# Kernel tuning notes

Measured on AMD Instinct MI355X. Metric: run time of the kernel, lower is better.

## Reference

```python
import jax, jax.numpy as jnp
import numpy as np

D_MODEL = 1024
NUM_HEADS = 16
D_K = D_MODEL // NUM_HEADS


def setup_inputs() -> dict:
    key = jax.random.key(0)
    ks = jax.random.split(key, 8)
    B, S = 2, 2048
    std = 1.0 / np.sqrt(D_MODEL)
    return {
        "Q": jax.random.normal(ks[0], (B, S, D_MODEL), jnp.float32),
        "K": jax.random.normal(ks[1], (B, S, D_MODEL), jnp.float32),
        "V": jax.random.normal(ks[2], (B, S, D_MODEL), jnp.float32),
        "W_q": jax.random.normal(ks[3], (D_MODEL, D_MODEL), jnp.float32) * std,
        "W_k": jax.random.normal(ks[4], (D_MODEL, D_MODEL), jnp.float32) * std,
        "W_v": jax.random.normal(ks[5], (D_MODEL, D_MODEL), jnp.float32) * std,
        "W_o": jax.random.normal(ks[6], (D_MODEL, D_MODEL), jnp.float32) * std,
        "b_o": jnp.zeros((D_MODEL,), jnp.float32),
    }


def reference(Q, K, V, W_q, W_k, W_v, W_o, b_o):
    B, S, _ = Q.shape
    H, dk = NUM_HEADS, D_K
    scale = 1.0 / np.sqrt(dk)
    # project and split heads: [B, H, S, dk]
    def split_heads(x, W):
        return (x @ W.T).reshape(B, -1, H, dk).transpose(0, 2, 1, 3)
    q = split_heads(Q, W_q)
    k = split_heads(K, W_k)
    v = split_heads(V, W_v)
    # scores: [B, H, S, S]
    scores = jnp.einsum("bhqd,bhkd->bhqk", q, k) * scale
    causal_mask = jnp.triu(jnp.ones((S, S), bool), k=1)
    scores = jnp.where(causal_mask, -jnp.inf, scores)
    attn = jax.nn.softmax(scores, axis=-1)
    out = jnp.einsum("bhqk,bhkd->bhqd", attn, v)  # [B, H, S, dk]
    out = out.transpose(0, 2, 1, 3).reshape(B, S, H * dk)
    out = out @ W_o.T + b_o
    return out, attn
```

## Files before the change

kernel.cpp:

```cpp
#include <hip/hip_runtime.h>
#include <hip/hip_bf16.h>

#define SEQ 2048
#define BATCH 2
#define NH 16
#define DK 64
#define DM 1024

typedef __bf16 bf16;
typedef __bf16 bf16x8 __attribute__((ext_vector_type(8)));
typedef float f32x4 __attribute__((ext_vector_type(4)));
typedef short s16x4 __attribute__((ext_vector_type(4)));

#define MFMA16(a,b,c) __builtin_amdgcn_mfma_f32_16x16x32_bf16(a,b,c,0,0,0)
#define NEG_BIG (-1.0e30f)

#define GLL16(gsrc, ldst) __builtin_amdgcn_global_load_lds( \
    (const __attribute__((address_space(1))) void*)(gsrc), \
    (__attribute__((address_space(3))) void*)(ldst), 16, 0, 0)

__device__ __forceinline__ bf16x8 ld8(const bf16* p){ return *(const bf16x8*)p; }

__device__ __forceinline__ bf16x8 frag_bf16lds(const bf16* Ls, int row, int lq){
    int c = lq ^ (row&3);
    return *(const bf16x8*)((const char*)Ls + row*64 + c*16);
}

__global__ __launch_bounds__(256) void cvt_kernel(
    const float* __restrict__ Q,  const float* __restrict__ K,  const float* __restrict__ V,
    const float* __restrict__ Wq, const float* __restrict__ Wk, const float* __restrict__ Wv,
    bf16* __restrict__ Qb, bf16* __restrict__ Kb, bf16* __restrict__ Vb,
    bf16* __restrict__ Wqb, bf16* __restrict__ Wkb, bf16* __restrict__ Wvb)
{
    const int a = blockIdx.y;
    const float* src = (a==0)?Q:(a==1)?K:(a==2)?V:(a==3)?Wq:(a==4)?Wk:Wv;
    bf16* dst        = (a==0)?Qb:(a==1)?Kb:(a==2)?Vb:(a==3)?Wqb:(a==4)?Wkb:Wvb;
    const int n4 = (a<3) ? (BATCH*SEQ*DM)/4 : (DM*DM)/4;
    for (int i = blockIdx.x*256 + threadIdx.x; i < n4; i += gridDim.x*256){
        f32x4 v = ((const f32x4*)src)[i];
        bf16 o[4];
        #pragma unroll
        for (int j=0;j<4;j++) o[j] = (bf16)v[j];
        ((s16x4*)dst)[i] = *(const s16x4*)o;
    }
}

__global__ __launch_bounds__(256) void cvtW_kernel(
    const float* __restrict__ W, bf16* __restrict__ Wb)
{
    const int n4 = (DM*DM)/4;
    for (int i = blockIdx.x*256 + threadIdx.x; i < n4; i += gridDim.x*256){
        f32x4 v = ((const f32x4*)W)[i];
        bf16 o[4];
        #pragma unroll
        for (int j=0;j<4;j++) o[j] = (bf16)v[j];
        ((s16x4*)Wb)[i] = *(const s16x4*)o;
    }
}

__device__ __forceinline__ void gemm_tile_bf16(
    const bf16* __restrict__ X, const bf16* __restrict__ W,
    bf16* As, bf16* Bs, int m0, int n0, int tid, int mt, int nt0,
    int lr, int lq, f32x4 acc[4][4])
{
    for (int k0 = 0; k0 < DM; k0 += 32) {
        if (k0) __syncthreads();
        #pragma unroll
        for (int i=0;i<2;i++){
            int ci  = i*256 + tid;
            int row = ci >> 2, ch = ci & 3;
            int gc  = (ch ^ (row&3)) << 3;
            GLL16(X + (size_t)(m0+row)*DM + k0 + gc, (char*)As + ci*16);
            GLL16(W + (size_t)(n0+row)*DM + k0 + gc, (char*)Bs + ci*16);
        }
        __syncthreads();
        bf16x8 af[4], bfr[4];
        #pragma unroll
        for (int mi=0;mi<4;mi++) af[mi]  = frag_bf16lds(As, mt  + mi*16 + lr, lq);
        #pragma unroll
        for (int ni=0;ni<4;ni++) bfr[ni] = frag_bf16lds(Bs, nt0 + ni*16 + lr, lq);
        #pragma unroll
        for (int mi=0;mi<4;mi++)
            #pragma unroll
            for (int ni=0;ni<4;ni++)
                acc[mi][ni] = MFMA16(af[mi], bfr[ni], acc[mi][ni]);
    }
}

__global__ __launch_bounds__(256) void qkv_proj_kernel(
    const bf16* __restrict__ Qb, const bf16* __restrict__ Kb, const bf16* __restrict__ Vb,
    const bf16* __restrict__ Wqb, const bf16* __restrict__ Wkb, const bf16* __restrict__ Wvb,
    bf16* __restrict__ q_s, bf16* __restrict__ k_s, bf16* __restrict__ vt_s)
{
    __shared__ __align__(16) bf16 As[128*32];
    __shared__ __align__(16) bf16 Bs[128*32];
    const int z = blockIdx.z;
    const bf16* X = (z==0) ? Qb  : (z==1) ? Kb  : Vb;
    const bf16* W = (z==0) ? Wqb : (z==1) ? Wkb : Wvb;
    bf16* out     = (z==0) ? q_s : (z==1) ? k_s : vt_s;

    const int tid  = threadIdx.x;
    const int lane = tid & 63;
    const int w    = tid >> 6;
    const int lr = lane & 15, lq = lane >> 4;
    const int mt  = (w>>1)*64;
    const int nt0 = (w&1)*64;
    const int m0 = blockIdx.y*128;
    const int n0 = blockIdx.x*128;

    f32x4 acc[4][4] = {};
    gemm_tile_bf16(X, W, As, Bs, m0, n0, tid, mt, nt0, lr, lq, acc);

    if (z == 2) {
        #pragma unroll
        for (int mi=0;mi<4;mi++)
        #pragma unroll
        for (int ni=0;ni<4;ni++){
            int row = m0 + mt + mi*16 + lq*4;
            int col = n0 + nt0 + ni*16 + lr;
            int b = row >> 11, s = row & (SEQ-1);
            int h = col >> 6,  dd = col & 63;
            bf16 pk[4];
            #pragma unroll
            for (int r=0;r<4;r++) pk[r] = (bf16)acc[mi][ni][r];
            *(s16x4*)&out[((size_t)((b*NH + h)*DK + dd))*SEQ + s] = *(const s16x4*)pk;
        }
    } else {
        #pragma unroll
        for (int mi=0;mi<4;mi++)
        #pragma unroll
        for (int ni=0;ni<4;ni++)
        #pragma unroll
        for (int r=0;r<4;r++) {
            int row = m0 + mt + mi*16 + lq*4 + r;
            int col = n0 + nt0 + ni*16 + lr;
            int b = row >> 11, s = row & (SEQ-1);
            int h = col >> 6,  dd = col & 63;
            out[((size_t)(b*NH + h))*SEQ*DK + (size_t)s*DK + dd] = (bf16)acc[mi][ni][r];
        }
    }
}

__device__ __forceinline__ void load_ktile(const bf16* __restrict__ kp,
                                           int kt, int lr, int lq, bf16x8* kf){
    #pragma unroll
    for (int ks=0;ks<2;ks++)
        #pragma unroll
        for (int nt=0;nt<4;nt++)
            kf[ks*4+nt] = ld8(kp + (size_t)(kt*64 + nt*16 + lr)*DK + ks*32 + lq*8);
}

__device__ __forceinline__ void mfma_scores(const bf16x8* qf, const bf16x8* kf, f32x4* s){
    const f32x4 z4 = {0.f,0.f,0.f,0.f};
    #pragma unroll
    for (int nt=0;nt<4;nt++) s[nt] = z4;
    #pragma unroll
    for (int ks=0;ks<2;ks++)
        #pragma unroll
        for (int nt=0;nt<4;nt++)
            s[nt] = MFMA16(qf[ks], kf[ks*4+nt], s[nt]);
}

__global__ __launch_bounds__(128,2) void attn_kernel(
    const bf16* __restrict__ q_s, const bf16* __restrict__ k_s,
    const bf16* __restrict__ vt_s,
    float* __restrict__ attn_out, bf16* __restrict__ ao)
{
    __shared__ __align__(16) bf16 P[2][32][64];
    const int bh = blockIdx.x;
    const int lane = threadIdx.x & 63, w = threadIdx.x >> 6;
    const int lr = lane & 15, lq = lane >> 4;
    const int qtile = w ? (63 - (int)blockIdx.y) : (int)blockIdx.y;
    const int qw0   = qtile*32;
    const int ktmax = (qw0 + 31) >> 6;

    const bf16* qp = q_s  + (size_t)bh*SEQ*DK;
    const bf16* kp = k_s  + (size_t)bh*SEQ*DK;
    const bf16* vp = vt_s + (size_t)bh*DK*SEQ;
    float* ab = attn_out + (size_t)bh*SEQ*SEQ;
    char* Pw = (char*)&P[w][0][0];

    bf16x8 qf[2][2];
    #pragma unroll
    for (int qi=0;qi<2;qi++)
        #pragma unroll
        for (int ks=0;ks<2;ks++)
            qf[qi][ks] = ld8(qp + (size_t)(qw0+qi*16+lr)*DK + ks*32 + lq*8);

    float lsum[2][4] = {};
    bf16x8 kf[8];
    load_ktile(kp, 0, lr, lq, kf);
    for (int kt=0; kt<ktmax; kt++) {
        bf16x8 kn[8];
        load_ktile(kp, kt+1, lr, lq, kn);
        #pragma unroll
        for (int qi=0;qi<2;qi++){
            f32x4 s[4];
            mfma_scores(qf[qi], kf, s);
            #pragma unroll
            for (int nt=0;nt<4;nt++)
                #pragma unroll
                for (int r=0;r<4;r++)
                    lsum[qi][r] += __expf(s[nt][r]*0.125f);
        }
        #pragma unroll
        for (int i=0;i<8;i++) kf[i] = kn[i];
    }
    {
        #pragma unroll
        for (int qi=0;qi<2;qi++){
            f32x4 s[4];
            mfma_scores(qf[qi], kf, s);
            #pragma unroll
            for (int nt=0;nt<4;nt++)
                #pragma unroll
                for (int r=0;r<4;r++){
                    float v = s[nt][r]*0.125f;
                    if ((ktmax*64 + nt*16 + lr) > (qw0 + qi*16 + lq*4 + r)) v = NEG_BIG;
                    lsum[qi][r] += __expf(v);
                }
        }
    }
    float inv_l[2][4];
    #pragma unroll
    for (int qi=0;qi<2;qi++)
        #pragma unroll
        for (int r=0;r<4;r++){
            float t = lsum[qi][r];
            t += __shfl_xor(t,1); t += __shfl_xor(t,2);
            t += __shfl_xor(t,4); t += __shfl_xor(t,8);
            inv_l[qi][r] = 1.0f / t;
        }

    f32x4 o[2][4] = {};
    for (int kt=0; kt<=ktmax; kt++) {
        load_ktile(kp, kt, lr, lq, kf);
        bf16x8 vf[8];
        #pragma unroll
        for (int ks=0;ks<2;ks++)
            #pragma unroll
            for (int nt=0;nt<4;nt++)
                vf[ks*4+nt] = ld8(vp + (size_t)(nt*16+lr)*SEQ + kt*64 + ks*32 + lq*8);
        #pragma unroll
        for (int qi=0;qi<2;qi++){
            f32x4 s[4];
            mfma_scores(qf[qi], kf, s);
            if (kt < ktmax) {
                #pragma unroll
                for (int nt=0;nt<4;nt++)
                    #pragma unroll
                    for (int r=0;r<4;r++){
                        float p = __expf(s[nt][r]*0.125f) * inv_l[qi][r];
                        int row = qi*16 + lq*4 + r, col = nt*16 + lr;
                        ab[(size_t)(qw0 + row)*SEQ + kt*64 + col] = p;
                        *(bf16*)(Pw + row*128 + ((col*2) ^ ((row&7)<<4))) = (bf16)p;
                    }
            } else {
                #pragma unroll
                for (int nt=0;nt<4;nt++)
                    #pragma unroll
                    for (int r=0;r<4;r++){
                        float v = s[nt][r]*0.125f;
                        if ((kt*64 + nt*16 + lr) > (qw0 + qi*16 + lq*4 + r)) v = NEG_BIG;
                        float p = __expf(v) * inv_l[qi][r];
                        int row = qi*16 + lq*4 + r, col = nt*16 + lr;
                        ab[(size_t)(qw0 + row)*SEQ + kt*64 + col] = p;
                        *(bf16*)(Pw + row*128 + ((col*2) ^ ((row&7)<<4))) = (bf16)p;
                    }
            }
        }
        __asm__ __volatile__("" ::: "memory");
        #pragma unroll
        for (int qi=0;qi<2;qi++)
            #pragma unroll
            for (int ks=0;ks<2;ks++){
                int row = qi*16 + lr;
                bf16x8 pf = *(const bf16x8*)(Pw + row*128
                                + ((ks*64 + lq*16) ^ ((row&7)<<4)));
                #pragma unroll
                for (int nt=0;nt<4;nt++)
                    o[qi][nt] = MFMA16(pf, vf[ks*4+nt], o[qi][nt]);
            }
    }

    const int b = bh >> 4, h = bh & 15;
    #pragma unroll
    for (int qi=0;qi<2;qi++)
        #pragma unroll
        for (int nt=0;nt<4;nt++)
            #pragma unroll
            for (int r=0;r<4;r++){
                int qrow = qw0 + qi*16 + lq*4 + r;
                ao[(size_t)(b*SEQ + qrow)*DM + h*64 + nt*16 + lr] = (bf16)o[qi][nt][r];
            }

    int cstart = (ktmax+1)*64;
    if (cstart < SEQ) {
        const f32x4 z4 = {0.f,0.f,0.f,0.f};
        float* rp = ab + (size_t)(qw0 + (lane>>1))*SEQ;
        for (int c4 = (cstart>>2) + (lane&1); c4 < (SEQ>>2); c4 += 2)
            *(f32x4*)(rp + c4*4) = z4;
    }
}

__global__ __launch_bounds__(256) void out_proj_kernel(
    const bf16* __restrict__ Xa, const bf16* __restrict__ Wob,
    const float* __restrict__ bo, float* __restrict__ out)
{
    __shared__ __align__(16) bf16 As[128*32];
    __shared__ __align__(16) bf16 Bs[128*32];
    const int tid  = threadIdx.x;
    const int lane = tid & 63;
    const int w    = tid >> 6;
    const int lr = lane & 15, lq = lane >> 4;
    const int mt  = (w>>1)*64;
    const int nt0 = (w&1)*64;
    const int m0 = blockIdx.y*128;
    const int n0 = blockIdx.x*128;

    f32x4 acc[4][4] = {};
    gemm_tile_bf16(Xa, Wob, As, Bs, m0, n0, tid, mt, nt0, lr, lq, acc);

    #pragma unroll
    for (int mi=0;mi<4;mi++)
    #pragma unroll
    for (int ni=0;ni<4;ni++)
    #pragma unroll
    for (int r=0;r<4;r++) {
        int row = m0 + mt + mi*16 + lq*4 + r;
        int col = n0 + nt0 + ni*16 + lr;
        out[(size_t)row*DM + col] = acc[mi][ni][r] + bo[col];
    }
}

extern "C" void kernel_launch(void* const* d_in, const int* in_sizes, int n_in,
                              void* d_out, int out_size, void* d_ws, size_t ws_size,
                              hipStream_t stream)
{
    const float* Q  = (const float*)d_in[0];
    const float* K  = (const float*)d_in[1];
    const float* V  = (const float*)d_in[2];
    const float* Wq = (const float*)d_in[3];
    const float* Wk = (const float*)d_in[4];
    const float* Wv = (const float*)d_in[5];
    const float* Wo = (const float*)d_in[6];
    const float* bo = (const float*)d_in[7];
    float* out = (float*)d_out;

    bf16* ws = (bf16*)d_ws;
    const size_t NTOK = (size_t)BATCH*SEQ*DM;
    bf16* q_s  = ws;
    bf16* k_s  = ws + NTOK;
    bf16* vt_s = ws + 2*NTOK;
    bf16* ao   = ws + 3*NTOK;

    float* ab  = out + NTOK;
    bf16* Qb   = (bf16*)ab;
    bf16* Kb   = Qb + NTOK;
    bf16* Vb   = Qb + 2*NTOK;
    bf16* Wqb  = Qb + 3*NTOK;
    bf16* Wkb  = Wqb + (size_t)DM*DM;
    bf16* Wvb  = Wqb + 2*(size_t)DM*DM;

    bf16* Wob  = q_s;

    cvt_kernel<<<dim3(256,6), 256, 0, stream>>>(Q,K,V,Wq,Wk,Wv, Qb,Kb,Vb,Wqb,Wkb,Wvb);
    qkv_proj_kernel<<<dim3(8,32,3), 256, 0, stream>>>(Qb,Kb,Vb,Wqb,Wkb,Wvb, q_s,k_s,vt_s);
    attn_kernel<<<dim3(32,32), 128, 0, stream>>>(q_s,k_s,vt_s, ab, ao);
    cvtW_kernel<<<dim3(128), 256, 0, stream>>>(Wo, Wob);
    out_proj_kernel<<<dim3(8,32), 256, 0, stream>>>(ao,Wob,bo,out);
}
```

Before: 763.1 us.

## Double-buffer GEMM tiles, remap block order, stage V-transpose via LDS, pipeline attention K loads

The projection GEMMs now double-buffer their LDS tiles so the global-to-LDS loads for the next K-slab overlap the MFMAs on the current one. Block indices are remapped so consecutive blocks walk along M, which changes L2 reuse of the weight tiles. The V-transpose epilogue goes through LDS and writes 16-byte coalesced stores instead of scattered 8-byte ones. The attention kernel unrolls its K loop by two with ping-pong register buffers, prefetches K across both passes, and uses exp2 with the log2e factor folded into the scale. The cost is double the LDS per GEMM block and higher register pressure in attention, which may reduce occupancy.

```diff
diff --git a/kernel.cpp b/kernel.cpp
--- a/kernel.cpp
+++ b/kernel.cpp
@@ -14,6 +14,7 @@
 
 #define MFMA16(a,b,c) __builtin_amdgcn_mfma_f32_16x16x32_bf16(a,b,c,0,0,0)
 #define NEG_BIG (-1.0e30f)
+#define SC_LOG2E 0.18033688011112042f
 
 #define GLL16(gsrc, ldst) __builtin_amdgcn_global_load_lds( \
     (const __attribute__((address_space(1))) void*)(gsrc), \
@@ -58,32 +59,47 @@
     }
 }
 
-__device__ __forceinline__ void gemm_tile_bf16(
+__device__ __forceinline__ void stage_tiles(
     const bf16* __restrict__ X, const bf16* __restrict__ W,
-    bf16* As, bf16* Bs, int m0, int n0, int tid, int mt, int nt0,
+    bf16* As, bf16* Bs, int m0, int n0, int k0, int tid)
+{
+    #pragma unroll
+    for (int i=0;i<2;i++){
+        int ci  = i*256 + tid;
+        int row = ci >> 2, ch = ci & 3;
+        int gc  = (ch ^ (row&3)) << 3;
+        GLL16(X + (size_t)(m0+row)*DM + k0 + gc, (char*)As + ci*16);
+        GLL16(W + (size_t)(n0+row)*DM + k0 + gc, (char*)Bs + ci*16);
+    }
+}
+
+__device__ __forceinline__ void gemm_tile_db(
+    const bf16* __restrict__ X, const bf16* __restrict__ W,
+    char* lds, int m0, int n0, int tid, int mt, int nt0,
     int lr, int lq, f32x4 acc[4][4])
 {
+    bf16* As0 = (bf16*)(lds);
+    bf16* Bs0 = (bf16*)(lds + 8192);
+    bf16* As1 = (bf16*)(lds + 16384);
+    bf16* Bs1 = (bf16*)(lds + 24576);
+    stage_tiles(X, W, As0, Bs0, m0, n0, 0, tid);
+    __syncthreads();
     for (int k0 = 0; k0 < DM; k0 += 32) {
-        if (k0) __syncthreads();
-        #pragma unroll
-        for (int i=0;i<2;i++){
-            int ci  = i*256 + tid;
-            int row = ci >> 2, ch = ci & 3;
-            int gc  = (ch ^ (row&3)) << 3;
-            GLL16(X + (size_t)(m0+row)*DM + k0 + gc, (char*)As + ci*16);
-            GLL16(W + (size_t)(n0+row)*DM + k0 + gc, (char*)Bs + ci*16);
-        }
-        __syncthreads();
+        bf16 *Ac, *Bc, *An, *Bn;
+        if ((k0>>5)&1){ Ac=As1; Bc=Bs1; An=As0; Bn=Bs0; }
+        else          { Ac=As0; Bc=Bs0; An=As1; Bn=Bs1; }
+        if (k0+32 < DM) stage_tiles(X, W, An, Bn, m0, n0, k0+32, tid);
         bf16x8 af[4], bfr[4];
         #pragma unroll
-        for (int mi=0;mi<4;mi++) af[mi]  = frag_bf16lds(As, mt  + mi*16 + lr, lq);
-        #pragma unroll
-        for (int ni=0;ni<4;ni++) bfr[ni] = frag_bf16lds(Bs, nt0 + ni*16 + lr, lq);
+        for (int mi=0;mi<4;mi++) af[mi]  = frag_bf16lds(Ac, mt  + mi*16 + lr, lq);
+        #pragma unroll
+        for (int ni=0;ni<4;ni++) bfr[ni] = frag_bf16lds(Bc, nt0 + ni*16 + lr, lq);
         #pragma unroll
         for (int mi=0;mi<4;mi++)
             #pragma unroll
             for (int ni=0;ni<4;ni++)
                 acc[mi][ni] = MFMA16(af[mi], bfr[ni], acc[mi][ni]);
+        __syncthreads();
     }
 }
 
@@ -92,8 +108,7 @@
     const bf16* __restrict__ Wqb, const bf16* __restrict__ Wkb, const bf16* __restrict__ Wvb,
     bf16* __restrict__ q_s, bf16* __restrict__ k_s, bf16* __restrict__ vt_s)
 {
-    __shared__ __align__(16) bf16 As[128*32];
-    __shared__ __align__(16) bf16 Bs[128*32];
+    __shared__ __align__(16) char lds[32768];
     const int z = blockIdx.z;
     const bf16* X = (z==0) ? Qb  : (z==1) ? Kb  : Vb;
     const bf16* W = (z==0) ? Wqb : (z==1) ? Wkb : Wvb;
@@ -105,25 +120,37 @@
     const int lr = lane & 15, lq = lane >> 4;
     const int mt  = (w>>1)*64;
     const int nt0 = (w&1)*64;
-    const int m0 = blockIdx.y*128;
-    const int n0 = blockIdx.x*128;
+    const int flat = blockIdx.x + 8*blockIdx.y;
+    const int m0 = (flat & 31) * 128;
+    const int n0 = (flat >> 5) * 128;
 
     f32x4 acc[4][4] = {};
-    gemm_tile_bf16(X, W, As, Bs, m0, n0, tid, mt, nt0, lr, lq, acc);
+    gemm_tile_db(X, W, lds, m0, n0, tid, mt, nt0, lr, lq, acc);
 
     if (z == 2) {
+        __syncthreads();
         #pragma unroll
         for (int mi=0;mi<4;mi++)
         #pragma unroll
         for (int ni=0;ni<4;ni++){
-            int row = m0 + mt + mi*16 + lq*4;
-            int col = n0 + nt0 + ni*16 + lr;
-            int b = row >> 11, s = row & (SEQ-1);
-            int h = col >> 6,  dd = col & 63;
+            int col  = nt0 + ni*16 + lr;
+            int row0 = mt + mi*16 + lq*4;
             bf16 pk[4];
             #pragma unroll
             for (int r=0;r<4;r++) pk[r] = (bf16)acc[mi][ni][r];
-            *(s16x4*)&out[((size_t)((b*NH + h)*DK + dd))*SEQ + s] = *(const s16x4*)pk;
+            char* dst = lds + col*256 + (((row0>>3) ^ (col&15))<<4) + (row0&7)*2;
+            *(s16x4*)dst = *(const s16x4*)pk;
+        }
+        __syncthreads();
+        const int b = m0 >> 11, srow0 = m0 & (SEQ-1);
+        #pragma unroll
+        for (int j=0;j<8;j++){
+            int col = j*16 + (tid>>4);
+            int sc  = tid & 15;
+            bf16x8 val = *(const bf16x8*)(lds + col*256 + ((sc ^ (col&15))<<4));
+            int gcol = n0 + col;
+            int h = gcol>>6, dd = gcol&63;
+            *(bf16x8*)&out[((size_t)((b*NH+h)*DK+dd))*SEQ + srow0 + sc*8] = val;
         }
     } else {
         #pragma unroll
@@ -150,6 +177,15 @@
             kf[ks*4+nt] = ld8(kp + (size_t)(kt*64 + nt*16 + lr)*DK + ks*32 + lq*8);
 }
 
+__device__ __forceinline__ void load_vtile(const bf16* __restrict__ vp,
+                                           int kt, int lr, int lq, bf16x8* vf){
+    #pragma unroll
+    for (int ks=0;ks<2;ks++)
+        #pragma unroll
+        for (int nt=0;nt<4;nt++)
+            vf[ks*4+nt] = ld8(vp + (size_t)(nt*16+lr)*SEQ + kt*64 + ks*32 + lq*8);
+}
+
 __device__ __forceinline__ void mfma_scores(const bf16x8* qf, const bf16x8* kf, f32x4* s){
     const f32x4 z4 = {0.f,0.f,0.f,0.f};
     #pragma unroll
@@ -159,6 +195,63 @@
         #pragma unroll
         for (int nt=0;nt<4;nt++)
             s[nt] = MFMA16(qf[ks], kf[ks*4+nt], s[nt]);
+}
+
+#define P1_TILE(KT, KC, KN)                                                  \
+{                                                                            \
+    const int _kt = (KT);                                                    \
+    if (_kt < ktmax) load_ktile(kp, _kt+1, lr, lq, (KN));                    \
+    _Pragma("unroll")                                                        \
+    for (int qi=0;qi<2;qi++){                                                \
+        f32x4 s[4];                                                          \
+        mfma_scores(qf[qi], (KC), s);                                        \
+        _Pragma("unroll")                                                    \
+        for (int nt=0;nt<4;nt++)                                             \
+            _Pragma("unroll")                                                \
+            for (int r=0;r<4;r++){                                           \
+                float v = s[nt][r]*SC_LOG2E;                                 \
+                if ((_kt*64 + nt*16 + lr) > (qw0 + qi*16 + lq*4 + r))        \
+                    v = NEG_BIG;                                             \
+                lsum[qi][r] += exp2f(v);                                     \
+            }                                                                \
+    }                                                                        \
+}
+
+#define P2_TILE(KT, KC, KN)                                                  \
+{                                                                            \
+    const int _kt = (KT);                                                    \
+    bf16x8 vf[8];                                                            \
+    load_vtile(vp, _kt, lr, lq, vf);                                         \
+    if (_kt < ktmax) load_ktile(kp, _kt+1, lr, lq, (KN));                    \
+    _Pragma("unroll")                                                        \
+    for (int qi=0;qi<2;qi++){                                                \
+        f32x4 s[4];                                                          \
+        mfma_scores(qf[qi], (KC), s);                                        \
+        _Pragma("unroll")                                                    \
+        for (int nt=0;nt<4;nt++)                                             \
+            _Pragma("unroll")                                                \
+            for (int r=0;r<4;r++){                                           \
+                float v = s[nt][r]*SC_LOG2E;                                 \
+                if ((_kt*64 + nt*16 + lr) > (qw0 + qi*16 + lq*4 + r))        \
+                    v = NEG_BIG;                                             \
+                float p = exp2f(v) * inv_l[qi][r];                           \
+                int row = qi*16 + lq*4 + r, col = nt*16 + lr;                \
+                ab[(size_t)(qw0 + row)*SEQ + _kt*64 + col] = p;              \
+                *(bf16*)(Pw + row*128 + ((col*2) ^ ((row&7)<<4))) = (bf16)p; \
+            }                                                                \
+    }                                                                        \
+    __asm__ __volatile__("" ::: "memory");                                   \
+    _Pragma("unroll")                                                        \
+    for (int qi=0;qi<2;qi++)                                                 \
+        _Pragma("unroll")                                                    \
+        for (int ks=0;ks<2;ks++){                                            \
+            int prow = qi*16 + lr;                                           \
+            bf16x8 pf = *(const bf16x8*)(Pw + prow*128 +                     \
+                            ((ks*64 + lq*16) ^ ((prow&7)<<4)));              \
+            _Pragma("unroll")                                                \
+            for (int nt=0;nt<4;nt++)                                         \
+                o[qi][nt] = MFMA16(pf, vf[ks*4+nt], o[qi][nt]);              \
+        }                                                                    \
 }
 
 __global__ __launch_bounds__(128,2) void attn_kernel(
@@ -187,39 +280,13 @@
         for (int ks=0;ks<2;ks++)
             qf[qi][ks] = ld8(qp + (size_t)(qw0+qi*16+lr)*DK + ks*32 + lq*8);
 
+    bf16x8 kA[8], kB[8];
     float lsum[2][4] = {};
-    bf16x8 kf[8];
-    load_ktile(kp, 0, lr, lq, kf);
-    for (int kt=0; kt<ktmax; kt++) {
-        bf16x8 kn[8];
-        load_ktile(kp, kt+1, lr, lq, kn);
-        #pragma unroll
-        for (int qi=0;qi<2;qi++){
-            f32x4 s[4];
-            mfma_scores(qf[qi], kf, s);
-            #pragma unroll
-            for (int nt=0;nt<4;nt++)
-                #pragma unroll
-                for (int r=0;r<4;r++)
-                    lsum[qi][r] += __expf(s[nt][r]*0.125f);
-        }
-        #pragma unroll
-        for (int i=0;i<8;i++) kf[i] = kn[i];
-    }
-    {
-        #pragma unroll
-        for (int qi=0;qi<2;qi++){
-            f32x4 s[4];
-            mfma_scores(qf[qi], kf, s);
-            #pragma unroll
-            for (int nt=0;nt<4;nt++)
-                #pragma unroll
-                for (int r=0;r<4;r++){
-                    float v = s[nt][r]*0.125f;
-                    if ((ktmax*64 + nt*16 + lr) > (qw0 + qi*16 + lq*4 + r)) v = NEG_BIG;
-                    lsum[qi][r] += __expf(v);
-                }
-        }
+
+    load_ktile(kp, 0, lr, lq, kA);
+    for (int kt=0; kt<=ktmax; kt+=2){
+        P1_TILE(kt, kA, kB);
+        if (kt+1 <= ktmax) P1_TILE(kt+1, kB, kA);
     }
     float inv_l[2][4];
     #pragma unroll
@@ -233,54 +300,10 @@
         }
 
     f32x4 o[2][4] = {};
-    for (int kt=0; kt<=ktmax; kt++) {
-        load_ktile(kp, kt, lr, lq, kf);
-        bf16x8 vf[8];
-        #pragma unroll
-        for (int ks=0;ks<2;ks++)
-            #pragma unroll
-            for (int nt=0;nt<4;nt++)
-                vf[ks*4+nt] = ld8(vp + (size_t)(nt*16+lr)*SEQ + kt*64 + ks*32 + lq*8);
-        #pragma unroll
-        for (int qi=0;qi<2;qi++){
-            f32x4 s[4];
-            mfma_scores(qf[qi], kf, s);
-            if (kt < ktmax) {
-                #pragma unroll
-                for (int nt=0;nt<4;nt++)
-                    #pragma unroll
-                    for (int r=0;r<4;r++){
-                        float p = __expf(s[nt][r]*0.125f) * inv_l[qi][r];
-                        int row = qi*16 + lq*4 + r, col = nt*16 + lr;
-                        ab[(size_t)(qw0 + row)*SEQ + kt*64 + col] = p;
-                        *(bf16*)(Pw + row*128 + ((col*2) ^ ((row&7)<<4))) = (bf16)p;
-                    }
-            } else {
-                #pragma unroll
-                for (int nt=0;nt<4;nt++)
-                    #pragma unroll
-                    for (int r=0;r<4;r++){
-                        float v = s[nt][r]*0.125f;
-                        if ((kt*64 + nt*16 + lr) > (qw0 + qi*16 + lq*4 + r)) v = NEG_BIG;
-                        float p = __expf(v) * inv_l[qi][r];
-                        int row = qi*16 + lq*4 + r, col = nt*16 + lr;
-                        ab[(size_t)(qw0 + row)*SEQ + kt*64 + col] = p;
-                        *(bf16*)(Pw + row*128 + ((col*2) ^ ((row&7)<<4))) = (bf16)p;
-                    }
-            }
-        }
-        __asm__ __volatile__("" ::: "memory");
-        #pragma unroll
-        for (int qi=0;qi<2;qi++)
-            #pragma unroll
-            for (int ks=0;ks<2;ks++){
-                int row = qi*16 + lr;
-                bf16x8 pf = *(const bf16x8*)(Pw + row*128
-                                + ((ks*64 + lq*16) ^ ((row&7)<<4)));
-                #pragma unroll
-                for (int nt=0;nt<4;nt++)
-                    o[qi][nt] = MFMA16(pf, vf[ks*4+nt], o[qi][nt]);
-            }
+    load_ktile(kp, 0, lr, lq, kA);
+    for (int kt=0; kt<=ktmax; kt+=2){
+        P2_TILE(kt, kA, kB);
+        if (kt+1 <= ktmax) P2_TILE(kt+1, kB, kA);
     }
 
     const int b = bh >> 4, h = bh & 15;
@@ -307,19 +330,19 @@
     const bf16* __restrict__ Xa, const bf16* __restrict__ Wob,
     const float* __restrict__ bo, float* __restrict__ out)
 {
-    __shared__ __align__(16) bf16 As[128*32];
-    __shared__ __align__(16) bf16 Bs[128*32];
+    __shared__ __align__(16) char lds[32768];
     const int tid  = threadIdx.x;
     const int lane = tid & 63;
     const int w    = tid >> 6;
     const int lr = lane & 15, lq = lane >> 4;
     const int mt  = (w>>1)*64;
     const int nt0 = (w&1)*64;
-    const int m0 = blockIdx.y*128;
-    const int n0 = blockIdx.x*128;
+    const int flat = blockIdx.x + 8*blockIdx.y;
+    const int m0 = (flat & 31) * 128;
+    const int n0 = (flat >> 5) * 128;
 
     f32x4 acc[4][4] = {};
-    gemm_tile_bf16(Xa, Wob, As, Bs, m0, n0, tid, mt, nt0, lr, lq, acc);
+    gemm_tile_db(Xa, Wob, lds, m0, n0, tid, mt, nt0, lr, lq, acc);
 
     #pragma unroll
     for (int mi=0;mi<4;mi++)
```

After: 880.4 us. 15.4% more time.
